# Performance work log

Measured on AMD Instinct MI355X. Metric: run time of the kernel, lower is better.

The kernel has to match this reference:

```python
import jax, jax.numpy as jnp
import numpy as np

B, T, D, L, E = 8, 2048, 256, 8, 64


def setup_inputs() -> dict:
    key = jax.random.key(0)
    ks = jax.random.split(key, 5)
    x = jax.random.normal(ks[0], (B, T, D), dtype=jnp.float32)
    # MMLP params: weight (4L, D, E), bias (4L, E); nn.Linear: (2L, D), (2L,)
    W_ml = jax.random.normal(ks[1], (4 * L, D, E), dtype=jnp.float32) * 0.05
    b_ml = jax.random.normal(ks[2], (4 * L, E), dtype=jnp.float32) * 0.05
    W_lin = jax.random.normal(ks[3], (2 * L, D), dtype=jnp.float32) * 0.05
    b_lin = jax.random.normal(ks[4], (2 * L,), dtype=jnp.float32) * 0.05
    return {"x": x, "W_ml": W_ml, "b_ml": b_ml, "W_lin": W_lin, "b_lin": b_lin}


def _xlstm_forward(x, W_ml, b_ml, W_lin, b_lin):
    b, t, _ = x.shape
    l4, _, e = W_ml.shape
    l = l4 // 4
    # Precompute all per-step gate projections at once (the torch code does this per step).
    mg = jnp.einsum('bti,lij->btlj', x, W_ml) + b_ml          # (B,T,4L,E)
    lg = jnp.einsum('bti,li->btl', x, W_lin) + b_lin          # (B,T,2L)
    o_, v, k, q = jnp.split(mg, 4, axis=2)                    # each (B,T,L,E)
    i_, f_ = jnp.split(lg, 2, axis=2)                         # each (B,T,L)
    xs = tuple(jnp.moveaxis(a, 1, 0) for a in (o_, v, k, q, i_, f_))  # time-major

    def step(carry, inp):
        m, n, C, h = carry
        o_t, v_t, k_t, q_t, i_t, f_t = inp
        m_new = jnp.maximum(f_t + m, i_t)                     # stabilizer (B,L)
        i_g = jnp.exp(i_t - m_new)
        f_g = jnp.exp(f_t + m - m_new)
        # rank-1 outer-product update of matrix cell state (B,L,E,E)
        C = f_g[:, :, None, None] * C + i_g[:, :, None, None] * (v_t[:, :, :, None] * k_t[:, :, None, :])
        n = f_g[:, :, None] * n + i_g[:, :, None] * k_t       # (B,L,E)
        denom = jnp.maximum(jnp.sum(n * q_t, axis=-1), 1.0)[:, :, None]  # clamp(.,1,inf)
        h = jax.nn.sigmoid(o_t) * jnp.einsum('blij,bli->blj', C, q_t) / denom
        return (m_new, n, C, h), None

    init = (
        jnp.zeros((b, l), jnp.float32),
        jnp.zeros((b, l, e), jnp.float32),
        jnp.zeros((b, l, e, e), jnp.float32),
        jnp.zeros((b, l, e), jnp.float32),
    )
    (m, n, C, h), _ = jax.lax.scan(step, init, xs)
    return h, C


def reference(x, W_ml, b_ml, W_lin, b_lin):
    return _xlstm_forward(x, W_ml, b_ml, W_lin, b_lin)
```

## Files before the change

kernel.cpp:

```cpp
#include <hip/hip_runtime.h>

#define B 8
#define T 2048
#define D 256
#define L 8
#define E 64
#define BT (B*T)

typedef _Float16 f16;
typedef f16 f16x8 __attribute__((ext_vector_type(8)));
typedef float f32x4 __attribute__((ext_vector_type(4)));

#define OFF_I   0
#define OFF_F   (OFF_I  + B*L*T)
#define OFF_WT  (OFF_F  + B*L*T)
#define OFF_VT  (OFF_WT + 16*E*D/2)
#define OFF_KT  (OFF_VT + B*L*E*T/2)
#define OFF_CP  (OFF_KT + B*L*E*T/2)
#define OFF_X16 (OFF_CP + 64*4*4160)

__global__ __launch_bounds__(256) void k_prep_all(const float* __restrict__ x,
        const float* __restrict__ Wlin, const float* __restrict__ blin,
        const float* __restrict__ Wml,
        float* __restrict__ ibuf, float* __restrict__ fbuf,
        f16* __restrict__ Wt16, f16* __restrict__ x16) {
    __shared__ __align__(16) char smem[49920];
    int tid = threadIdx.x;
    int bx = blockIdx.x;
    if (bx < 512) {
        float (*xs)[260] = (float(*)[260])smem;
        float (*wsm)[260] = (float(*)[260])(smem + 33280);
        int t0 = bx * 32;
        {
            int row = tid >> 3, q = tid & 7;
            const float* src = x + (size_t)(t0 + row) * D + q * 32;
            #pragma unroll
            for (int j = 0; j < 8; ++j) {
                float4 v = *(const float4*)(src + j * 4);
                *(float4*)&xs[row][q * 32 + j * 4] = v;
            }
        }
        {
            int row = tid >> 4, c0 = (tid & 15) * 16;
            const float* src = Wlin + row * D + c0;
            #pragma unroll
            for (int j = 0; j < 4; ++j) {
                float4 v = *(const float4*)(src + j * 4);
                *(float4*)&wsm[row][c0 + j * 4] = v;
            }
        }
        __syncthreads();
        int tl = tid >> 4, g = tid & 15;
        float acc0 = 0.f, acc1 = 0.f;
        for (int i = 0; i < D; ++i) {
            float wv = wsm[g][i];
            acc0 += xs[tl * 2 + 0][i] * wv;
            acc1 += xs[tl * 2 + 1][i] * wv;
        }
        float bias = blin[g];
        float acc[2] = {acc0 + bias, acc1 + bias};
        #pragma unroll
        for (int u = 0; u < 2; ++u) {
            int t = t0 + tl * 2 + u;
            int b = t >> 11, tt = t & 2047;
            if (g < 8) ibuf[(b * L + g) * T + tt] = acc[u];
            else       fbuf[(b * L + (g - 8)) * T + tt] = acc[u];
        }
    } else if (bx < 528) {
        float (*ts)[65] = (float(*)[65])smem;
        int vkrow = bx - 512;
        int wrow = 8 + vkrow;
        for (int dc = 0; dc < 4; ++dc) {
            int d0 = dc * 64;
            int r = tid >> 2, cq = (tid & 3) * 16;
            const float* src = Wml + ((size_t)wrow * D + d0 + r) * E + cq;
            #pragma unroll
            for (int j = 0; j < 16; j += 4) {
                float4 v = *(const float4*)(src + j);
                ts[r][cq + j] = v.x; ts[r][cq + j + 1] = v.y;
                ts[r][cq + j + 2] = v.z; ts[r][cq + j + 3] = v.w;
            }
            __syncthreads();
            int e = tid >> 2, dq = (tid & 3) * 16;
            f16* dst = Wt16 + ((size_t)vkrow * E + e) * D + d0 + dq;
            f16x8 o0, o1;
            #pragma unroll
            for (int j = 0; j < 8; ++j) {
                o0[j] = (f16)ts[dq + j][e];
                o1[j] = (f16)ts[dq + 8 + j][e];
            }
            *(f16x8*)dst = o0;
            *(f16x8*)(dst + 8) = o1;
            __syncthreads();
        }
    } else {
        int i = ((bx - 528) * 256 + tid) * 8;
        float4 v0 = *(const float4*)(x + i);
        float4 v1 = *(const float4*)(x + i + 4);
        f16x8 o;
        o[0] = (f16)v0.x; o[1] = (f16)v0.y; o[2] = (f16)v0.z; o[3] = (f16)v0.w;
        o[4] = (f16)v1.x; o[5] = (f16)v1.y; o[6] = (f16)v1.z; o[7] = (f16)v1.w;
        *(f16x8*)(x16 + i) = o;
    }
}

__global__ __launch_bounds__(512) void k_vkproj3(const f16* __restrict__ x16,
        const f16* __restrict__ Wt16, const float* __restrict__ bml,
        f16* __restrict__ Vt, f16* __restrict__ Kt) {
    __shared__ __align__(16) char lds[40960];
    int tid = threadIdx.x;
    int bx = blockIdx.x, h = blockIdx.y;
    int t0 = bx * 128;
    const f16* xa = x16 + (size_t)t0 * D;
    const f16* wb = Wt16 + (size_t)h * 8 * E * D;
    int wv = tid >> 6, lane = tid & 63;
    int wr = wv >> 2, wc = wv & 3;
    int q = lane >> 4, lr = lane & 15;
    int sa_t = tid >> 2, sa_q = tid & 3;
    f32x4 acc[4][8] = {};
    for (int ks = 0; ks < 8; ++ks) {
        int k0 = ks * 32;
        {
            f16x8 v = *(const f16x8*)(xa + (size_t)sa_t * D + k0 + sa_q * 8);
            int ba = sa_t * 64 + ((sa_q ^ ((sa_t >> 1) & 3)) << 4);
            *(f16x8*)(lds + ba) = v;
        }
        #pragma unroll
        for (int rr = 0; rr < 4; ++rr) {
            int r = rr * 128 + (tid >> 2);
            int c = tid & 3;
            f16x8 v = *(const f16x8*)(wb + (size_t)r * D + k0 + c * 8);
            int ba = 8192 + r * 64 + ((c ^ ((r >> 1) & 3)) << 4);
            *(f16x8*)(lds + ba) = v;
        }
        __syncthreads();
        f16x8 a[4], bf[8];
        #pragma unroll
        for (int m = 0; m < 4; ++m) {
            int t = wr * 64 + m * 16 + lr;
            int ba = t * 64 + ((q ^ ((t >> 1) & 3)) << 4);
            a[m] = *(const f16x8*)(lds + ba);
        }
        #pragma unroll
        for (int n = 0; n < 8; ++n) {
            int c = wc * 128 + n * 16 + lr;
            int ba = 8192 + c * 64 + ((q ^ ((c >> 1) & 3)) << 4);
            bf[n] = *(const f16x8*)(lds + ba);
        }
        #pragma unroll
        for (int m = 0; m < 4; ++m)
            #pragma unroll
            for (int n = 0; n < 8; ++n)
                acc[m][n] = __builtin_amdgcn_mfma_f32_16x16x32_f16(
                    a[m], bf[n], acc[m][n], 0, 0, 0);
        __syncthreads();
    }
    const float* bp = bml + (size_t)(8 + h * 8) * E;
    int b_g = t0 >> 11, tin = t0 & 2047;
    f16* obase = h ? Kt : Vt;
    for (int p = 0; p < 4; ++p) {
        if (wc == p) {
            #pragma unroll
            for (int n = 0; n < 8; ++n) {
                int cc = n * 16 + lr;
                float bias = bp[p * 128 + cc];
                int swz = (cc & 7) << 4;
                #pragma unroll
                for (int m = 0; m < 4; ++m) {
                    #pragma unroll
                    for (int r = 0; r < 4; r += 2) {
                        int t = wr * 64 + m * 16 + q * 4 + r;
                        union { f16 h2[2]; unsigned u; } pk;
                        pk.h2[0] = (f16)(acc[m][n][r] + bias);
                        pk.h2[1] = (f16)(acc[m][n][r + 1] + bias);
                        int ba = cc * 256 + ((t * 2) ^ swz);
                        *(unsigned*)(lds + ba) = pk.u;
                    }
                }
            }
        }
        __syncthreads();
        {
            int cc = tid >> 2, part = tid & 3;
            int cg = p * 128 + cc;
            int l = cg >> 6, e = cg & 63;
            f16* dst = obase + ((size_t)((b_g * L + l) * E + e)) * T + tin + part * 32;
            int swz = (cc & 7) << 4;
            #pragma unroll
            for (int jj = 0; jj < 4; ++jj) {
                int t = part * 32 + jj * 8;
                int ba = cc * 256 + ((t * 2) ^ swz);
                *(f16x8*)(dst + jj * 8) = *(const f16x8*)(lds + ba);
            }
        }
        __syncthreads();
    }
}

__global__ __launch_bounds__(256) void k_cgemm2s(const f16* __restrict__ Vt,
        const f16* __restrict__ Kt, const float* __restrict__ ibuf,
        const float* __restrict__ fbuf, float* __restrict__ Cpart) {
    __shared__ float red[64 * 64];
    __shared__ float redn[64];
    __shared__ float part[256];
    __shared__ float rmax[256];
    __shared__ __align__(16) f16 wlds[512];
    int tid = threadIdx.x;
    int bl = blockIdx.x, tc = blockIdx.y;
    int wv = tid >> 6, lane = tid & 63;
    {
        const float* fp = fbuf + bl * T + tid * 8;
        const float* ip = ibuf + bl * T + tid * 8;
        float4 fa = *(const float4*)fp;
        float4 fb = *(const float4*)(fp + 4);
        float4 ia = *(const float4*)ip;
        float4 ib = *(const float4*)(ip + 4);
        float f[8] = {fa.x, fa.y, fa.z, fa.w, fb.x, fb.y, fb.z, fb.w};
        float iv[8] = {ia.x, ia.y, ia.z, ia.w, ib.x, ib.y, ib.z, ib.w};
        float ls[8]; float run = 0.f;
        #pragma unroll
        for (int r = 0; r < 8; ++r) { run += f[r]; ls[r] = run; }
        part[tid] = run;
        __syncthreads();
        float inc = run;
        #pragma unroll
        for (int s = 1; s < 256; s <<= 1) {
            float u = (tid >= s) ? part[tid - s] : 0.f;
            __syncthreads();
            inc += u;
            part[tid] = inc;
            __syncthreads();
        }
        float off = inc - run;
        float e[8]; float lmax = -1e30f;
        #pragma unroll
        for (int r = 0; r < 8; ++r) { e[r] = iv[r] - (off + ls[r]); lmax = fmaxf(lmax, e[r]); }
        rmax[tid] = lmax;
        __syncthreads();
        for (int s = 128; s > 0; s >>= 1) {
            if (tid < s) rmax[tid] = fmaxf(rmax[tid], rmax[tid + s]);
            __syncthreads();
        }
        float M = fmaxf(rmax[0], 0.0f);
        int t = tid * 8;
        if ((t >> 9) == tc) {
            f16x8 w8;
            #pragma unroll
            for (int r = 0; r < 8; ++r) w8[r] = (f16)__expf(e[r] - M);
            *(f16x8*)&wlds[t & 511] = w8;
        }
        __syncthreads();
    }
    const f16* vp = Vt + (size_t)bl * E * T;
    const f16* kp = Kt + (size_t)bl * E * T;
    f32x4 acc[5][4] = {};
    int tbase = tc * 512 + wv * 128;
    for (int kc = 0; kc < 4; ++kc) {
        int tt = tbase + kc * 32 + (lane >> 4) * 8;
        f16x8 wfrag = *(const f16x8*)&wlds[tt & 511];
        f16x8 a[5], bf[4];
        #pragma unroll
        for (int m = 0; m < 4; ++m) {
            int i = m * 16 + (lane & 15);
            f16x8 v = *(const f16x8*)(vp + (size_t)i * T + tt);
            a[m] = v * wfrag;
        }
        a[4] = wfrag;
        #pragma unroll
        for (int nn = 0; nn < 4; ++nn) {
            int j = nn * 16 + (lane & 15);
            bf[nn] = *(const f16x8*)(kp + (size_t)j * T + tt);
        }
        #pragma unroll
        for (int m = 0; m < 5; ++m)
            #pragma unroll
            for (int nn = 0; nn < 4; ++nn)
                acc[m][nn] = __builtin_amdgcn_mfma_f32_16x16x32_f16(
                    a[m], bf[nn], acc[m][nn], 0, 0, 0);
    }
    for (int rr = 0; rr < 4; ++rr) {
        if (wv == rr) {
            #pragma unroll
            for (int m = 0; m < 4; ++m)
                #pragma unroll
                for (int nn = 0; nn < 4; ++nn)
                    #pragma unroll
                    for (int r = 0; r < 4; ++r) {
                        int row = m * 16 + (lane >> 4) * 4 + r;
                        int col = nn * 16 + (lane & 15);
                        if (rr == 0) red[row * 64 + col] = acc[m][nn][r];
                        else         red[row * 64 + col] += acc[m][nn][r];
                    }
            if ((lane >> 4) == 0) {
                #pragma unroll
                for (int nn = 0; nn < 4; ++nn) {
                    int col = nn * 16 + (lane & 15);
                    if (rr == 0) redn[col] = acc[4][nn][0];
                    else         redn[col] += acc[4][nn][0];
                }
            }
        }
        __syncthreads();
    }
    float* cp = Cpart + ((size_t)bl * 4 + tc) * 4160;
    #pragma unroll
    for (int j = 0; j < 4; ++j) {
        int idx = tid * 16 + j * 4;
        *(float4*)(cp + idx) = *(const float4*)(red + idx);
    }
    if (tid < 64) cp[4096 + tid] = redn[tid];
}

__global__ __launch_bounds__(256) void k_final(const float* __restrict__ x,
        const float* __restrict__ Wml, const float* __restrict__ bml,
        const float* __restrict__ Cpart, float* __restrict__ out) {
    __shared__ float Cs[E * E];
    __shared__ float xs[D];
    __shared__ float ns[E];
    __shared__ float os[E];
    __shared__ float qs[E];
    int tid = threadIdx.x;
    int bl = blockIdx.x; int b = bl >> 3, l = bl & 7;
    xs[tid] = x[((size_t)(b * T + (T - 1))) * D + tid];
    const float* cp = Cpart + (size_t)bl * 4 * 4160;
    #pragma unroll
    for (int j = 0; j < 4; ++j) {
        int idx = tid * 16 + j * 4;
        float4 s = {0, 0, 0, 0};
        #pragma unroll
        for (int p = 0; p < 4; ++p) {
            float4 v = *(const float4*)(cp + p * 4160 + idx);
            s.x += v.x; s.y += v.y; s.z += v.z; s.w += v.w;
        }
        *(float4*)&Cs[idx] = s;
        *(float4*)(out + 4096 + (size_t)bl * (E * E) + idx) = s;
    }
    if (tid < 64) {
        float s = 0.f;
        #pragma unroll
        for (int p = 0; p < 4; ++p) s += cp[p * 4160 + 4096 + tid];
        ns[tid] = s;
    }
    __syncthreads();
    if (tid < 128) {
        int gate = tid >> 6, e = tid & 63;
        int wrow = gate ? (3 * L + l) : l;
        const float* wpp = Wml + (size_t)wrow * D * E + e;
        float s = 0.f;
        for (int kk = 0; kk < D; ++kk) s += xs[kk] * wpp[kk * E];
        s += bml[wrow * E + e];
        if (gate) qs[e] = s; else os[e] = s;
    }
    __syncthreads();
    if (tid < 64) {
        int j = tid;
        float hc = 0.f;
        for (int i2 = 0; i2 < E; ++i2) hc += Cs[i2 * E + j] * qs[i2];
        float nq = 0.f;
        for (int i2 = 0; i2 < E; ++i2) nq += ns[i2] * qs[i2];
        float denom = fmaxf(nq, 1.0f);
        float sg = 1.0f / (1.0f + __expf(-os[j]));
        out[bl * E + j] = sg * hc / denom;
    }
}

extern "C" void kernel_launch(void* const* d_in, const int* in_sizes, int n_in,
                              void* d_out, int out_size, void* d_ws, size_t ws_size,
                              hipStream_t stream) {
    const float* x    = (const float*)d_in[0];
    const float* Wml  = (const float*)d_in[1];
    const float* bml  = (const float*)d_in[2];
    const float* Wlin = (const float*)d_in[3];
    const float* blin = (const float*)d_in[4];
    float* out = (float*)d_out;
    float* ws = (float*)d_ws;
    float* ibuf  = ws + OFF_I;
    float* fbuf  = ws + OFF_F;
    f16*   Wt16  = (f16*)(ws + OFF_WT);
    f16*   Vt    = (f16*)(ws + OFF_VT);
    f16*   Kt    = (f16*)(ws + OFF_KT);
    float* Cpart = ws + OFF_CP;
    f16*   x16   = (f16*)(ws + OFF_X16);

    k_prep_all<<<2576, 256, 0, stream>>>(x, Wlin, blin, Wml, ibuf, fbuf, Wt16, x16);
    k_vkproj3<<<dim3(BT / 128, 2), 512, 0, stream>>>(x16, Wt16, bml, Vt, Kt);
    k_cgemm2s<<<dim3(B * L, 4), 256, 0, stream>>>(Vt, Kt, ibuf, fbuf, Cpart);
    k_final<<<B * L, 256, 0, stream>>>(x, Wml, bml, Cpart, out);
}
```

Before: 65.34 us.

## Fuse four kernels into one cooperative persistent kernel with grid syncs

Replaces the four-kernel pipeline (prep, V/K projection GEMM, chunked C GEMM, final reduction) with a single cooperative launch of 256 blocks of 512 threads, separated by grid-wide syncs. The o/q projection for the final step moves into the prep phase. The scan and C-GEMM phase is reorganised for 512 threads. The aim is to remove kernel launch gaps and tail effects across the small stages. In exchange it adds grid-barrier costs and fixes the occupancy to 256 blocks, which may underuse the GPU in the prep and GEMM phases.

Result: slower. 188.0 us (+187.7%).

```diff
diff --git a/kernel.cpp b/kernel.cpp
--- a/kernel.cpp
+++ b/kernel.cpp
@@ -1,4 +1,6 @@
 #include <hip/hip_runtime.h>
+#include <hip/hip_cooperative_groups.h>
+namespace cg = cooperative_groups;
 
 #define B 8
 #define T 2048
@@ -18,349 +20,361 @@
 #define OFF_KT  (OFF_VT + B*L*E*T/2)
 #define OFF_CP  (OFF_KT + B*L*E*T/2)
 #define OFF_X16 (OFF_CP + 64*4*4160)
-
-__global__ __launch_bounds__(256) void k_prep_all(const float* __restrict__ x,
-        const float* __restrict__ Wlin, const float* __restrict__ blin,
-        const float* __restrict__ Wml,
+#define OFF_OQ  (OFF_X16 + BT*D/2)
+
+__global__ __launch_bounds__(512, 2) void k_mega(
+        const float* __restrict__ x, const float* __restrict__ Wml,
+        const float* __restrict__ bml, const float* __restrict__ Wlin,
+        const float* __restrict__ blin, float* __restrict__ out,
         float* __restrict__ ibuf, float* __restrict__ fbuf,
-        f16* __restrict__ Wt16, f16* __restrict__ x16) {
+        f16* __restrict__ Wt16, f16* __restrict__ Vt, f16* __restrict__ Kt,
+        float* __restrict__ Cpart, f16* __restrict__ x16,
+        float* __restrict__ oqbuf) {
     __shared__ __align__(16) char smem[49920];
+    cg::grid_group grid = cg::this_grid();
     int tid = threadIdx.x;
-    int bx = blockIdx.x;
-    if (bx < 512) {
+    int bid = blockIdx.x;
+
+    {
         float (*xs)[260] = (float(*)[260])smem;
-        float (*wsm)[260] = (float(*)[260])(smem + 33280);
-        int t0 = bx * 32;
+        float (*wl)[260] = (float(*)[260])(smem + 33280);
         {
-            int row = tid >> 3, q = tid & 7;
-            const float* src = x + (size_t)(t0 + row) * D + q * 32;
-            #pragma unroll
-            for (int j = 0; j < 8; ++j) {
-                float4 v = *(const float4*)(src + j * 4);
-                *(float4*)&xs[row][q * 32 + j * 4] = v;
-            }
-        }
-        {
-            int row = tid >> 4, c0 = (tid & 15) * 16;
-            const float* src = Wlin + row * D + c0;
-            #pragma unroll
-            for (int j = 0; j < 4; ++j) {
-                float4 v = *(const float4*)(src + j * 4);
-                *(float4*)&wsm[row][c0 + j * 4] = v;
-            }
-        }
-        __syncthreads();
-        int tl = tid >> 4, g = tid & 15;
-        float acc0 = 0.f, acc1 = 0.f;
-        for (int i = 0; i < D; ++i) {
-            float wv = wsm[g][i];
-            acc0 += xs[tl * 2 + 0][i] * wv;
-            acc1 += xs[tl * 2 + 1][i] * wv;
-        }
-        float bias = blin[g];
-        float acc[2] = {acc0 + bias, acc1 + bias};
+            int row = tid >> 5, c = (tid & 31) * 8;
+            const float* src = Wlin + row * D + c;
+            float4 v0 = *(const float4*)src, v1 = *(const float4*)(src + 4);
+            *(float4*)&wl[row][c] = v0; *(float4*)&wl[row][c + 4] = v1;
+        }
         #pragma unroll
         for (int u = 0; u < 2; ++u) {
-            int t = t0 + tl * 2 + u;
-            int b = t >> 11, tt = t & 2047;
-            if (g < 8) ibuf[(b * L + g) * T + tt] = acc[u];
-            else       fbuf[(b * L + (g - 8)) * T + tt] = acc[u];
-        }
-    } else if (bx < 528) {
-        float (*ts)[65] = (float(*)[65])smem;
-        int vkrow = bx - 512;
-        int wrow = 8 + vkrow;
-        for (int dc = 0; dc < 4; ++dc) {
-            int d0 = dc * 64;
-            int r = tid >> 2, cq = (tid & 3) * 16;
+            int t0 = bid * 64 + u * 32;
+            int row = tid >> 4, q = (tid & 15) * 16;
+            const float* src = x + (size_t)(t0 + row) * D + q;
+            float4 a0 = *(const float4*)src;
+            float4 a1 = *(const float4*)(src + 4);
+            float4 a2 = *(const float4*)(src + 8);
+            float4 a3 = *(const float4*)(src + 12);
+            __syncthreads();
+            *(float4*)&xs[row][q] = a0;
+            *(float4*)&xs[row][q + 4] = a1;
+            *(float4*)&xs[row][q + 8] = a2;
+            *(float4*)&xs[row][q + 12] = a3;
+            f16x8 h0, h1;
+            h0[0]=(f16)a0.x; h0[1]=(f16)a0.y; h0[2]=(f16)a0.z; h0[3]=(f16)a0.w;
+            h0[4]=(f16)a1.x; h0[5]=(f16)a1.y; h0[6]=(f16)a1.z; h0[7]=(f16)a1.w;
+            h1[0]=(f16)a2.x; h1[1]=(f16)a2.y; h1[2]=(f16)a2.z; h1[3]=(f16)a2.w;
+            h1[4]=(f16)a3.x; h1[5]=(f16)a3.y; h1[6]=(f16)a3.z; h1[7]=(f16)a3.w;
+            *(f16x8*)(x16 + (size_t)(t0 + row) * D + q) = h0;
+            *(f16x8*)(x16 + (size_t)(t0 + row) * D + q + 8) = h1;
+            __syncthreads();
+            int tt = tid >> 4, g = tid & 15;
+            float acc = 0.f;
+            for (int d = 0; d < D; d += 4) {
+                float4 xv = *(const float4*)&xs[tt][d];
+                float4 wv = *(const float4*)&wl[g][d];
+                acc += xv.x * wv.x + xv.y * wv.y + xv.z * wv.z + xv.w * wv.w;
+            }
+            acc += blin[g];
+            int t = t0 + tt; int b = t >> 11, trem = t & 2047;
+            if (g < 8) ibuf[(b * L + g) * T + trem] = acc;
+            else       fbuf[(b * L + (g - 8)) * T + trem] = acc;
+        }
+        if (bid < 64) {
+            __syncthreads();
+            float (*ts)[65] = (float(*)[65])smem;
+            int vkrow = bid >> 2, dc = bid & 3;
+            int wrow = 8 + vkrow, d0 = dc * 64;
+            int r = tid >> 3, cq = (tid & 7) * 8;
             const float* src = Wml + ((size_t)wrow * D + d0 + r) * E + cq;
-            #pragma unroll
-            for (int j = 0; j < 16; j += 4) {
-                float4 v = *(const float4*)(src + j);
-                ts[r][cq + j] = v.x; ts[r][cq + j + 1] = v.y;
-                ts[r][cq + j + 2] = v.z; ts[r][cq + j + 3] = v.w;
-            }
-            __syncthreads();
-            int e = tid >> 2, dq = (tid & 3) * 16;
-            f16* dst = Wt16 + ((size_t)vkrow * E + e) * D + d0 + dq;
-            f16x8 o0, o1;
-            #pragma unroll
-            for (int j = 0; j < 8; ++j) {
-                o0[j] = (f16)ts[dq + j][e];
-                o1[j] = (f16)ts[dq + 8 + j][e];
-            }
-            *(f16x8*)dst = o0;
-            *(f16x8*)(dst + 8) = o1;
-            __syncthreads();
-        }
-    } else {
-        int i = ((bx - 528) * 256 + tid) * 8;
-        float4 v0 = *(const float4*)(x + i);
-        float4 v1 = *(const float4*)(x + i + 4);
-        f16x8 o;
-        o[0] = (f16)v0.x; o[1] = (f16)v0.y; o[2] = (f16)v0.z; o[3] = (f16)v0.w;
-        o[4] = (f16)v1.x; o[5] = (f16)v1.y; o[6] = (f16)v1.z; o[7] = (f16)v1.w;
-        *(f16x8*)(x16 + i) = o;
+            float4 v0 = *(const float4*)src, v1 = *(const float4*)(src + 4);
+            *(float4*)&ts[r][cq] = v0; *(float4*)&ts[r][cq + 4] = v1;
+            __syncthreads();
+            int e = tid >> 3, dq = (tid & 7) * 8;
+            f16x8 o;
+            #pragma unroll
+            for (int j = 0; j < 8; ++j) o[j] = (f16)ts[dq + j][e];
+            *(f16x8*)(Wt16 + ((size_t)vkrow * E + e) * D + d0 + dq) = o;
+        } else if (bid < 72) {
+            __syncthreads();
+            float (*x8)[256] = (float(*)[256])smem;
+            int l = bid - 64;
+            {
+                int bb = tid >> 6, c = (tid & 63) * 4;
+                float4 v = *(const float4*)(x + ((size_t)(bb * T + (T - 1))) * D + c);
+                *(float4*)&x8[bb][c] = v;
+            }
+            __syncthreads();
+            #pragma unroll
+            for (int r = 0; r < 2; ++r) {
+                int idx = r * 512 + tid;
+                int gate = idx >> 9, b = (idx >> 6) & 7, e = idx & 63;
+                int row = gate ? (24 + l) : l;
+                const float* gp = Wml + (size_t)row * D * E + e;
+                float s = 0.f;
+                for (int kk = 0; kk < D; ++kk) s += x8[b][kk] * gp[(size_t)kk * E];
+                s += bml[row * E + e];
+                oqbuf[(b * L + l) * 128 + gate * 64 + e] = s;
+            }
+        }
     }
-}
-
-__global__ __launch_bounds__(512) void k_vkproj3(const f16* __restrict__ x16,
-        const f16* __restrict__ Wt16, const float* __restrict__ bml,
-        f16* __restrict__ Vt, f16* __restrict__ Kt) {
-    __shared__ __align__(16) char lds[40960];
-    int tid = threadIdx.x;
-    int bx = blockIdx.x, h = blockIdx.y;
-    int t0 = bx * 128;
-    const f16* xa = x16 + (size_t)t0 * D;
-    const f16* wb = Wt16 + (size_t)h * 8 * E * D;
-    int wv = tid >> 6, lane = tid & 63;
-    int wr = wv >> 2, wc = wv & 3;
-    int q = lane >> 4, lr = lane & 15;
-    int sa_t = tid >> 2, sa_q = tid & 3;
-    f32x4 acc[4][8] = {};
-    for (int ks = 0; ks < 8; ++ks) {
-        int k0 = ks * 32;
-        {
-            f16x8 v = *(const f16x8*)(xa + (size_t)sa_t * D + k0 + sa_q * 8);
-            int ba = sa_t * 64 + ((sa_q ^ ((sa_t >> 1) & 3)) << 4);
-            *(f16x8*)(lds + ba) = v;
-        }
-        #pragma unroll
-        for (int rr = 0; rr < 4; ++rr) {
-            int r = rr * 128 + (tid >> 2);
-            int c = tid & 3;
-            f16x8 v = *(const f16x8*)(wb + (size_t)r * D + k0 + c * 8);
-            int ba = 8192 + r * 64 + ((c ^ ((r >> 1) & 3)) << 4);
-            *(f16x8*)(lds + ba) = v;
-        }
-        __syncthreads();
-        f16x8 a[4], bf[8];
-        #pragma unroll
-        for (int m = 0; m < 4; ++m) {
-            int t = wr * 64 + m * 16 + lr;
-            int ba = t * 64 + ((q ^ ((t >> 1) & 3)) << 4);
-            a[m] = *(const f16x8*)(lds + ba);
-        }
-        #pragma unroll
-        for (int n = 0; n < 8; ++n) {
-            int c = wc * 128 + n * 16 + lr;
-            int ba = 8192 + c * 64 + ((q ^ ((c >> 1) & 3)) << 4);
-            bf[n] = *(const f16x8*)(lds + ba);
-        }
-        #pragma unroll
-        for (int m = 0; m < 4; ++m)
-            #pragma unroll
-            for (int n = 0; n < 8; ++n)
-                acc[m][n] = __builtin_amdgcn_mfma_f32_16x16x32_f16(
-                    a[m], bf[n], acc[m][n], 0, 0, 0);
-        __syncthreads();
-    }
-    const float* bp = bml + (size_t)(8 + h * 8) * E;
-    int b_g = t0 >> 11, tin = t0 & 2047;
-    f16* obase = h ? Kt : Vt;
-    for (int p = 0; p < 4; ++p) {
-        if (wc == p) {
+    grid.sync();
+
+    {
+        char* lds = smem;
+        int bx = bid & 127, h = bid >> 7;
+        int t0 = bx * 128;
+        const f16* xa = x16 + (size_t)t0 * D;
+        const f16* wb = Wt16 + (size_t)h * 8 * E * D;
+        int wv = tid >> 6, lane = tid & 63;
+        int wr = wv >> 2, wc = wv & 3;
+        int q = lane >> 4, lr = lane & 15;
+        int sa_t = tid >> 2, sa_q = tid & 3;
+        f32x4 acc[4][8] = {};
+        for (int ks = 0; ks < 8; ++ks) {
+            int k0 = ks * 32;
+            {
+                f16x8 v = *(const f16x8*)(xa + (size_t)sa_t * D + k0 + sa_q * 8);
+                int ba = sa_t * 64 + ((sa_q ^ ((sa_t >> 1) & 3)) << 4);
+                *(f16x8*)(lds + ba) = v;
+            }
+            #pragma unroll
+            for (int rr = 0; rr < 4; ++rr) {
+                int r = rr * 128 + (tid >> 2);
+                int c = tid & 3;
+                f16x8 v = *(const f16x8*)(wb + (size_t)r * D + k0 + c * 8);
+                int ba = 8192 + r * 64 + ((c ^ ((r >> 1) & 3)) << 4);
+                *(f16x8*)(lds + ba) = v;
+            }
+            __syncthreads();
+            f16x8 a[4], bf[8];
+            #pragma unroll
+            for (int m = 0; m < 4; ++m) {
+                int t = wr * 64 + m * 16 + lr;
+                int ba = t * 64 + ((q ^ ((t >> 1) & 3)) << 4);
+                a[m] = *(const f16x8*)(lds + ba);
+            }
             #pragma unroll
             for (int n = 0; n < 8; ++n) {
-                int cc = n * 16 + lr;
-                float bias = bp[p * 128 + cc];
-                int swz = (cc & 7) << 4;
-                #pragma unroll
-                for (int m = 0; m < 4; ++m) {
+                int c = wc * 128 + n * 16 + lr;
+                int ba = 8192 + c * 64 + ((q ^ ((c >> 1) & 3)) << 4);
+                bf[n] = *(const f16x8*)(lds + ba);
+            }
+            #pragma unroll
+            for (int m = 0; m < 4; ++m)
+                #pragma unroll
+                for (int n = 0; n < 8; ++n)
+                    acc[m][n] = __builtin_amdgcn_mfma_f32_16x16x32_f16(
+                        a[m], bf[n], acc[m][n], 0, 0, 0);
+            __syncthreads();
+        }
+        const float* bp = bml + (size_t)(8 + h * 8) * E;
+        int b_g = t0 >> 11, tin = t0 & 2047;
+        f16* obase = h ? Kt : Vt;
+        for (int p = 0; p < 4; ++p) {
+            if (wc == p) {
+                #pragma unroll
+                for (int n = 0; n < 8; ++n) {
+                    int cc = n * 16 + lr;
+                    float bias = bp[p * 128 + cc];
+                    int swz = (cc & 7) << 4;
                     #pragma unroll
-                    for (int r = 0; r < 4; r += 2) {
-                        int t = wr * 64 + m * 16 + q * 4 + r;
-                        union { f16 h2[2]; unsigned u; } pk;
-                        pk.h2[0] = (f16)(acc[m][n][r] + bias);
-                        pk.h2[1] = (f16)(acc[m][n][r + 1] + bias);
-                        int ba = cc * 256 + ((t * 2) ^ swz);
-                        *(unsigned*)(lds + ba) = pk.u;
+                    for (int m = 0; m < 4; ++m) {
+                        #pragma unroll
+                        for (int r = 0; r < 4; r += 2) {
+                            int t = wr * 64 + m * 16 + q * 4 + r;
+                            union { f16 h2[2]; unsigned u; } pk;
+                            pk.h2[0] = (f16)(acc[m][n][r] + bias);
+                            pk.h2[1] = (f16)(acc[m][n][r + 1] + bias);
+                            int ba = cc * 256 + ((t * 2) ^ swz);
+                            *(unsigned*)(lds + ba) = pk.u;
+                        }
                     }
                 }
             }
-        }
-        __syncthreads();
+            __syncthreads();
+            {
+                int cc = tid >> 2, part = tid & 3;
+                int cg2 = p * 128 + cc;
+                int l = cg2 >> 6, e = cg2 & 63;
+                f16* dst = obase + ((size_t)((b_g * L + l) * E + e)) * T + tin + part * 32;
+                int swz = (cc & 7) << 4;
+                #pragma unroll
+                for (int jj = 0; jj < 4; ++jj) {
+                    int t = part * 32 + jj * 8;
+                    int ba = cc * 256 + ((t * 2) ^ swz);
+                    *(f16x8*)(dst + jj * 8) = *(const f16x8*)(lds + ba);
+                }
+            }
+            __syncthreads();
+        }
+    }
+    grid.sync();
+
+    {
+        int bl = bid >> 2, tc = bid & 3;
+        float* red0  = (float*)smem;
+        float* red1  = (float*)(smem + 16384);
+        float* part  = (float*)(smem + 32768);
+        float* rmax  = (float*)(smem + 34816);
+        f16*   wlds  = (f16*)(smem + 36864);
+        float* redn0 = (float*)(smem + 37888);
+        float* redn1 = (float*)(smem + 38144);
         {
-            int cc = tid >> 2, part = tid & 3;
-            int cg = p * 128 + cc;
-            int l = cg >> 6, e = cg & 63;
-            f16* dst = obase + ((size_t)((b_g * L + l) * E + e)) * T + tin + part * 32;
-            int swz = (cc & 7) << 4;
-            #pragma unroll
-            for (int jj = 0; jj < 4; ++jj) {
-                int t = part * 32 + jj * 8;
-                int ba = cc * 256 + ((t * 2) ^ swz);
-                *(f16x8*)(dst + jj * 8) = *(const f16x8*)(lds + ba);
-            }
-        }
-        __syncthreads();
+            const float* fp = fbuf + bl * T + tid * 4;
+            const float* ip = ibuf + bl * T + tid * 4;
+            float4 fa = *(const float4*)fp;
+            float4 ia = *(const float4*)ip;
+            float f0[4] = {fa.x, fa.y, fa.z, fa.w};
+            float iv[4] = {ia.x, ia.y, ia.z, ia.w};
+            float ls[4]; float run = 0.f;
+            #pragma unroll
+            for (int r = 0; r < 4; ++r) { run += f0[r]; ls[r] = run; }
+            part[tid] = run;
+            __syncthreads();
+            float inc = run;
+            #pragma unroll
+            for (int s = 1; s < 512; s <<= 1) {
+                float uu = (tid >= s) ? part[tid - s] : 0.f;
+                __syncthreads();
+                inc += uu;
+                part[tid] = inc;
+                __syncthreads();
+            }
+            float off = inc - run;
+            float e[4]; float lmax = -1e30f;
+            #pragma unroll
+            for (int r = 0; r < 4; ++r) { e[r] = iv[r] - (off + ls[r]); lmax = fmaxf(lmax, e[r]); }
+            rmax[tid] = lmax;
+            __syncthreads();
+            for (int s = 256; s > 0; s >>= 1) {
+                if (tid < s) rmax[tid] = fmaxf(rmax[tid], rmax[tid + s]);
+                __syncthreads();
+            }
+            float M = fmaxf(rmax[0], 0.0f);
+            int tg = tid * 4;
+            if ((tg >> 9) == tc) {
+                union { f16 h[4]; unsigned long long u; } pw;
+                #pragma unroll
+                for (int r = 0; r < 4; ++r) pw.h[r] = (f16)__expf(e[r] - M);
+                *(unsigned long long*)&wlds[tg & 511] = pw.u;
+            }
+            __syncthreads();
+        }
+        int wv = tid >> 6, lane = tid & 63;
+        const f16* vp = Vt + (size_t)bl * E * T;
+        const f16* kp = Kt + (size_t)bl * E * T;
+        f32x4 acc[5][4] = {};
+        int tw = tc * 512 + wv * 64;
+        #pragma unroll
+        for (int kc = 0; kc < 2; ++kc) {
+            int lo = wv * 64 + kc * 32 + (lane >> 4) * 8;
+            int tt = tc * 512 + lo;
+            f16x8 wfrag = *(const f16x8*)&wlds[lo];
+            f16x8 a[5], bf[4];
+            #pragma unroll
+            for (int m = 0; m < 4; ++m) {
+                int i = m * 16 + (lane & 15);
+                f16x8 v = *(const f16x8*)(vp + (size_t)i * T + tt);
+                a[m] = v * wfrag;
+            }
+            a[4] = wfrag;
+            #pragma unroll
+            for (int nn = 0; nn < 4; ++nn) {
+                int j = nn * 16 + (lane & 15);
+                bf[nn] = *(const f16x8*)(kp + (size_t)j * T + tt);
+            }
+            #pragma unroll
+            for (int m = 0; m < 5; ++m)
+                #pragma unroll
+                for (int nn = 0; nn < 4; ++nn)
+                    acc[m][nn] = __builtin_amdgcn_mfma_f32_16x16x32_f16(
+                        a[m], bf[nn], acc[m][nn], 0, 0, 0);
+        }
+        (void)tw;
+        for (int rr = 0; rr < 4; ++rr) {
+            if (wv == rr || wv == rr + 4) {
+                float* rd = (wv < 4) ? red0 : red1;
+                float* rn = (wv < 4) ? redn0 : redn1;
+                #pragma unroll
+                for (int m = 0; m < 4; ++m)
+                    #pragma unroll
+                    for (int nn = 0; nn < 4; ++nn)
+                        #pragma unroll
+                        for (int r = 0; r < 4; ++r) {
+                            int row = m * 16 + (lane >> 4) * 4 + r;
+                            int col = nn * 16 + (lane & 15);
+                            if (rr == 0) rd[row * 64 + col] = acc[m][nn][r];
+                            else         rd[row * 64 + col] += acc[m][nn][r];
+                        }
+                if ((lane >> 4) == 0) {
+                    #pragma unroll
+                    for (int nn = 0; nn < 4; ++nn) {
+                        int col = nn * 16 + (lane & 15);
+                        if (rr == 0) rn[col] = acc[4][nn][0];
+                        else         rn[col] += acc[4][nn][0];
+                    }
+                }
+            }
+            __syncthreads();
+        }
+        float* cp = Cpart + ((size_t)bl * 4 + tc) * 4160;
+        int idx = tid * 8;
+        float4 s0, s1;
+        {
+            float4 a0 = *(const float4*)(red0 + idx);
+            float4 b0 = *(const float4*)(red1 + idx);
+            float4 a1 = *(const float4*)(red0 + idx + 4);
+            float4 b1 = *(const float4*)(red1 + idx + 4);
+            s0.x = a0.x + b0.x; s0.y = a0.y + b0.y; s0.z = a0.z + b0.z; s0.w = a0.w + b0.w;
+            s1.x = a1.x + b1.x; s1.y = a1.y + b1.y; s1.z = a1.z + b1.z; s1.w = a1.w + b1.w;
+        }
+        *(float4*)(cp + idx) = s0;
+        *(float4*)(cp + idx + 4) = s1;
+        if (tid < 64) cp[4096 + tid] = redn0[tid] + redn1[tid];
     }
-}
-
-__global__ __launch_bounds__(256) void k_cgemm2s(const f16* __restrict__ Vt,
-        const f16* __restrict__ Kt, const float* __restrict__ ibuf,
-        const float* __restrict__ fbuf, float* __restrict__ Cpart) {
-    __shared__ float red[64 * 64];
-    __shared__ float redn[64];
-    __shared__ float part[256];
-    __shared__ float rmax[256];
-    __shared__ __align__(16) f16 wlds[512];
-    int tid = threadIdx.x;
-    int bl = blockIdx.x, tc = blockIdx.y;
-    int wv = tid >> 6, lane = tid & 63;
-    {
-        const float* fp = fbuf + bl * T + tid * 8;
-        const float* ip = ibuf + bl * T + tid * 8;
-        float4 fa = *(const float4*)fp;
-        float4 fb = *(const float4*)(fp + 4);
-        float4 ia = *(const float4*)ip;
-        float4 ib = *(const float4*)(ip + 4);
-        float f[8] = {fa.x, fa.y, fa.z, fa.w, fb.x, fb.y, fb.z, fb.w};
-        float iv[8] = {ia.x, ia.y, ia.z, ia.w, ib.x, ib.y, ib.z, ib.w};
-        float ls[8]; float run = 0.f;
-        #pragma unroll
-        for (int r = 0; r < 8; ++r) { run += f[r]; ls[r] = run; }
-        part[tid] = run;
-        __syncthreads();
-        float inc = run;
-        #pragma unroll
-        for (int s = 1; s < 256; s <<= 1) {
-            float u = (tid >= s) ? part[tid - s] : 0.f;
-            __syncthreads();
-            inc += u;
-            part[tid] = inc;
-            __syncthreads();
-        }
-        float off = inc - run;
-        float e[8]; float lmax = -1e30f;
-        #pragma unroll
-        for (int r = 0; r < 8; ++r) { e[r] = iv[r] - (off + ls[r]); lmax = fmaxf(lmax, e[r]); }
-        rmax[tid] = lmax;
-        __syncthreads();
-        for (int s = 128; s > 0; s >>= 1) {
-            if (tid < s) rmax[tid] = fmaxf(rmax[tid], rmax[tid + s]);
-            __syncthreads();
-        }
-        float M = fmaxf(rmax[0], 0.0f);
-        int t = tid * 8;
-        if ((t >> 9) == tc) {
-            f16x8 w8;
-            #pragma unroll
-            for (int r = 0; r < 8; ++r) w8[r] = (f16)__expf(e[r] - M);
-            *(f16x8*)&wlds[t & 511] = w8;
-        }
-        __syncthreads();
-    }
-    const f16* vp = Vt + (size_t)bl * E * T;
-    const f16* kp = Kt + (size_t)bl * E * T;
-    f32x4 acc[5][4] = {};
-    int tbase = tc * 512 + wv * 128;
-    for (int kc = 0; kc < 4; ++kc) {
-        int tt = tbase + kc * 32 + (lane >> 4) * 8;
-        f16x8 wfrag = *(const f16x8*)&wlds[tt & 511];
-        f16x8 a[5], bf[4];
-        #pragma unroll
-        for (int m = 0; m < 4; ++m) {
-            int i = m * 16 + (lane & 15);
-            f16x8 v = *(const f16x8*)(vp + (size_t)i * T + tt);
-            a[m] = v * wfrag;
-        }
-        a[4] = wfrag;
-        #pragma unroll
-        for (int nn = 0; nn < 4; ++nn) {
-            int j = nn * 16 + (lane & 15);
-            bf[nn] = *(const f16x8*)(kp + (size_t)j * T + tt);
-        }
-        #pragma unroll
-        for (int m = 0; m < 5; ++m)
-            #pragma unroll
-            for (int nn = 0; nn < 4; ++nn)
-                acc[m][nn] = __builtin_amdgcn_mfma_f32_16x16x32_f16(
-                    a[m], bf[nn], acc[m][nn], 0, 0, 0);
-    }
-    for (int rr = 0; rr < 4; ++rr) {
-        if (wv == rr) {
-            #pragma unroll
-            for (int m = 0; m < 4; ++m)
-                #pragma unroll
-                for (int nn = 0; nn < 4; ++nn)
-                    #pragma unroll
-                    for (int r = 0; r < 4; ++r) {
-                        int row = m * 16 + (lane >> 4) * 4 + r;
-                        int col = nn * 16 + (lane & 15);
-                        if (rr == 0) red[row * 64 + col] = acc[m][nn][r];
-                        else         red[row * 64 + col] += acc[m][nn][r];
-                    }
-            if ((lane >> 4) == 0) {
-                #pragma unroll
-                for (int nn = 0; nn < 4; ++nn) {
-                    int col = nn * 16 + (lane & 15);
-                    if (rr == 0) redn[col] = acc[4][nn][0];
-                    else         redn[col] += acc[4][nn][0];
-                }
-            }
-        }
-        __syncthreads();
-    }
-    float* cp = Cpart + ((size_t)bl * 4 + tc) * 4160;
-    #pragma unroll
-    for (int j = 0; j < 4; ++j) {
-        int idx = tid * 16 + j * 4;
-        *(float4*)(cp + idx) = *(const float4*)(red + idx);
-    }
-    if (tid < 64) cp[4096 + tid] = redn[tid];
-}
-
-__global__ __launch_bounds__(256) void k_final(const float* __restrict__ x,
-        const float* __restrict__ Wml, const float* __restrict__ bml,
-        const float* __restrict__ Cpart, float* __restrict__ out) {
-    __shared__ float Cs[E * E];
-    __shared__ float xs[D];
-    __shared__ float ns[E];
-    __shared__ float os[E];
-    __shared__ float qs[E];
-    int tid = threadIdx.x;
-    int bl = blockIdx.x; int b = bl >> 3, l = bl & 7;
-    xs[tid] = x[((size_t)(b * T + (T - 1))) * D + tid];
-    const float* cp = Cpart + (size_t)bl * 4 * 4160;
-    #pragma unroll
-    for (int j = 0; j < 4; ++j) {
-        int idx = tid * 16 + j * 4;
-        float4 s = {0, 0, 0, 0};
+    grid.sync();
+
+    if (bid < 64) {
+        int bl = bid;
+        float* Cs  = (float*)smem;
+        float* ns  = (float*)(smem + 16384);
+        float* osb = (float*)(smem + 16640);
+        float* qsb = (float*)(smem + 16896);
+        const float* cp = Cpart + (size_t)bl * 4 * 4160;
+        int idx = tid * 8;
+        float4 s0 = {0,0,0,0}, s1 = {0,0,0,0};
         #pragma unroll
         for (int p = 0; p < 4; ++p) {
-            float4 v = *(const float4*)(cp + p * 4160 + idx);
-            s.x += v.x; s.y += v.y; s.z += v.z; s.w += v.w;
-        }
-        *(float4*)&Cs[idx] = s;
-        *(float4*)(out + 4096 + (size_t)bl * (E * E) + idx) = s;
-    }
-    if (tid < 64) {
-        float s = 0.f;
-        #pragma unroll
-        for (int p = 0; p < 4; ++p) s += cp[p * 4160 + 4096 + tid];
-        ns[tid] = s;
-    }
-    __syncthreads();
-    if (tid < 128) {
-        int gate = tid >> 6, e = tid & 63;
-        int wrow = gate ? (3 * L + l) : l;
-        const float* wpp = Wml + (size_t)wrow * D * E + e;
-        float s = 0.f;
-        for (int kk = 0; kk < D; ++kk) s += xs[kk] * wpp[kk * E];
-        s += bml[wrow * E + e];
-        if (gate) qs[e] = s; else os[e] = s;
-    }
-    __syncthreads();
-    if (tid < 64) {
-        int j = tid;
-        float hc = 0.f;
-        for (int i2 = 0; i2 < E; ++i2) hc += Cs[i2 * E + j] * qs[i2];
-        float nq = 0.f;
-        for (int i2 = 0; i2 < E; ++i2) nq += ns[i2] * qs[i2];
-        float denom = fmaxf(nq, 1.0f);
-        float sg = 1.0f / (1.0f + __expf(-os[j]));
-        out[bl * E + j] = sg * hc / denom;
+            float4 v0 = *(const float4*)(cp + p * 4160 + idx);
+            float4 v1 = *(const float4*)(cp + p * 4160 + idx + 4);
+            s0.x += v0.x; s0.y += v0.y; s0.z += v0.z; s0.w += v0.w;
+            s1.x += v1.x; s1.y += v1.y; s1.z += v1.z; s1.w += v1.w;
+        }
+        *(float4*)&Cs[idx] = s0;
+        *(float4*)&Cs[idx + 4] = s1;
+        *(float4*)(out + 4096 + (size_t)bl * 4096 + idx) = s0;
+        *(float4*)(out + 4096 + (size_t)bl * 4096 + idx + 4) = s1;
+        if (tid < 64) {
+            float s = 0.f;
+            #pragma unroll
+            for (int p = 0; p < 4; ++p) s += cp[p * 4160 + 4096 + tid];
+            ns[tid] = s;
+        }
+        if (tid < 128) {
+            float v = oqbuf[bl * 128 + tid];
+            if (tid < 64) osb[tid] = v; else qsb[tid - 64] = v;
+        }
+        __syncthreads();
+        if (tid < 64) {
+            int j = tid;
+            float hc = 0.f, nq = 0.f;
+            for (int i2 = 0; i2 < E; ++i2) {
+                hc += Cs[i2 * 64 + j] * qsb[i2];
+                nq += ns[i2] * qsb[i2];
+            }
+            float denom = fmaxf(nq, 1.0f);
+            float sg = 1.0f / (1.0f + __expf(-osb[j]));
+            out[bl * 64 + j] = sg * hc / denom;
+        }
     }
 }
 
@@ -381,9 +395,13 @@
     f16*   Kt    = (f16*)(ws + OFF_KT);
     float* Cpart = ws + OFF_CP;
     f16*   x16   = (f16*)(ws + OFF_X16);
-
-    k_prep_all<<<2576, 256, 0, stream>>>(x, Wlin, blin, Wml, ibuf, fbuf, Wt16, x16);
-    k_vkproj3<<<dim3(BT / 128, 2), 512, 0, stream>>>(x16, Wt16, bml, Vt, Kt);
-    k_cgemm2s<<<dim3(B * L, 4), 256, 0, stream>>>(Vt, Kt, ibuf, fbuf, Cpart);
-    k_final<<<B * L, 256, 0, stream>>>(x, Wml, bml, Cpart, out);
+    float* oqbuf = ws + OFF_OQ;
+
+    void* args[] = {
+        (void*)&x, (void*)&Wml, (void*)&bml, (void*)&Wlin, (void*)&blin,
+        (void*)&out, (void*)&ibuf, (void*)&fbuf, (void*)&Wt16,
+        (void*)&Vt, (void*)&Kt, (void*)&Cpart, (void*)&x16, (void*)&oqbuf
+    };
+    hipLaunchCooperativeKernel((void*)k_mega, dim3(256), dim3(512),
+                               args, 0, stream);
 }
```

## Fuse final readout into C-GEMM kernel and fold x16 conversion into prep

Applied to the files above, without the earlier changes.

Folds the fp16 conversion of x into the i/f-gate projection blocks, so the separate conversion blocks that re-read x are gone. The o/q projections for the last timestep move into 8 extra prep blocks. The separate final kernel is merged into the C-GEMM kernel, which now uses 64 blocks of 512 threads, each covering all of T, instead of 256 blocks writing partial sums to workspace. This removes one launch and the partial-sum round trip. In exchange the GEMM stage runs far fewer blocks on a large GPU, so each block does more serial work.

New measurement: 76.88 us. 17.7% more time.

```diff
diff --git a/kernel.cpp b/kernel.cpp
--- a/kernel.cpp
+++ b/kernel.cpp
@@ -16,14 +16,15 @@
 #define OFF_WT  (OFF_F  + B*L*T)
 #define OFF_VT  (OFF_WT + 16*E*D/2)
 #define OFF_KT  (OFF_VT + B*L*E*T/2)
-#define OFF_CP  (OFF_KT + B*L*E*T/2)
-#define OFF_X16 (OFF_CP + 64*4*4160)
-
-__global__ __launch_bounds__(256) void k_prep_all(const float* __restrict__ x,
+#define OFF_X16 (OFF_KT + B*L*E*T/2)
+#define OFF_OQ  (OFF_X16 + BT*D/2)
+
+__global__ __launch_bounds__(256) void k_prep(const float* __restrict__ x,
         const float* __restrict__ Wlin, const float* __restrict__ blin,
-        const float* __restrict__ Wml,
+        const float* __restrict__ Wml, const float* __restrict__ bml,
         float* __restrict__ ibuf, float* __restrict__ fbuf,
-        f16* __restrict__ Wt16, f16* __restrict__ x16) {
+        f16* __restrict__ Wt16, f16* __restrict__ x16,
+        float* __restrict__ oqbuf) {
     __shared__ __align__(16) char smem[49920];
     int tid = threadIdx.x;
     int bx = blockIdx.x;
@@ -32,12 +33,19 @@
         float (*wsm)[260] = (float(*)[260])(smem + 33280);
         int t0 = bx * 32;
         {
-            int row = tid >> 3, q = tid & 7;
-            const float* src = x + (size_t)(t0 + row) * D + q * 32;
-            #pragma unroll
-            for (int j = 0; j < 8; ++j) {
-                float4 v = *(const float4*)(src + j * 4);
-                *(float4*)&xs[row][q * 32 + j * 4] = v;
+            int row = tid >> 3, q = (tid & 7) * 32;
+            const float* src = x + (size_t)(t0 + row) * D + q;
+            f16* xdst = x16 + (size_t)(t0 + row) * D + q;
+            #pragma unroll
+            for (int j = 0; j < 4; ++j) {
+                float4 v0 = *(const float4*)(src + j * 8);
+                float4 v1 = *(const float4*)(src + j * 8 + 4);
+                *(float4*)&xs[row][q + j * 8] = v0;
+                *(float4*)&xs[row][q + j * 8 + 4] = v1;
+                f16x8 h;
+                h[0]=(f16)v0.x; h[1]=(f16)v0.y; h[2]=(f16)v0.z; h[3]=(f16)v0.w;
+                h[4]=(f16)v1.x; h[5]=(f16)v1.y; h[6]=(f16)v1.z; h[7]=(f16)v1.w;
+                *(f16x8*)(xdst + j * 8) = h;
             }
         }
         {
@@ -94,13 +102,27 @@
             __syncthreads();
         }
     } else {
-        int i = ((bx - 528) * 256 + tid) * 8;
-        float4 v0 = *(const float4*)(x + i);
-        float4 v1 = *(const float4*)(x + i + 4);
-        f16x8 o;
-        o[0] = (f16)v0.x; o[1] = (f16)v0.y; o[2] = (f16)v0.z; o[3] = (f16)v0.w;
-        o[4] = (f16)v1.x; o[5] = (f16)v1.y; o[6] = (f16)v1.z; o[7] = (f16)v1.w;
-        *(f16x8*)(x16 + i) = o;
+        float (*x8)[256] = (float(*)[256])smem;
+        int l = bx - 528;
+        {
+            int bb = tid >> 5, c = (tid & 31) * 8;
+            const float* src = x + ((size_t)(bb * T + (T - 1))) * D + c;
+            float4 v0 = *(const float4*)src, v1 = *(const float4*)(src + 4);
+            *(float4*)&x8[bb][c] = v0;
+            *(float4*)&x8[bb][c + 4] = v1;
+        }
+        __syncthreads();
+        #pragma unroll
+        for (int r = 0; r < 4; ++r) {
+            int idx = r * 256 + tid;
+            int gate = idx >> 9, b = (idx >> 6) & 7, e = idx & 63;
+            int row = gate ? (24 + l) : l;
+            const float* gp = Wml + (size_t)row * D * E + e;
+            float s = 0.f;
+            for (int kk = 0; kk < D; ++kk) s += x8[b][kk] * gp[(size_t)kk * E];
+            s += bml[row * E + e];
+            oqbuf[(b * L + l) * 128 + gate * 64 + e] = s;
+        }
     }
 }
 
@@ -182,8 +204,8 @@
         __syncthreads();
         {
             int cc = tid >> 2, part = tid & 3;
-            int cg = p * 128 + cc;
-            int l = cg >> 6, e = cg & 63;
+            int cg2 = p * 128 + cc;
+            int l = cg2 >> 6, e = cg2 & 63;
             f16* dst = obase + ((size_t)((b_g * L + l) * E + e)) * T + tin + part * 32;
             int swz = (cc & 7) << 4;
             #pragma unroll
@@ -197,67 +219,66 @@
     }
 }
 
-__global__ __launch_bounds__(256) void k_cgemm2s(const f16* __restrict__ Vt,
+__global__ __launch_bounds__(512) void k_cgemm_final(const f16* __restrict__ Vt,
         const f16* __restrict__ Kt, const float* __restrict__ ibuf,
-        const float* __restrict__ fbuf, float* __restrict__ Cpart) {
-    __shared__ float red[64 * 64];
-    __shared__ float redn[64];
-    __shared__ float part[256];
-    __shared__ float rmax[256];
-    __shared__ __align__(16) f16 wlds[512];
+        const float* __restrict__ fbuf, const float* __restrict__ oqbuf,
+        float* __restrict__ out) {
+    __shared__ __align__(16) char smem[41984];
+    float* red0  = (float*)smem;
+    float* red1  = (float*)(smem + 16384);
+    float* part  = (float*)(smem + 32768);
+    float* rmax  = (float*)(smem + 34816);
+    f16*   wlds  = (f16*)(smem + 36864);
+    float* redn0 = (float*)(smem + 40960);
+    float* redn1 = (float*)(smem + 41216);
     int tid = threadIdx.x;
-    int bl = blockIdx.x, tc = blockIdx.y;
+    int bl = blockIdx.x;
     int wv = tid >> 6, lane = tid & 63;
     {
-        const float* fp = fbuf + bl * T + tid * 8;
-        const float* ip = ibuf + bl * T + tid * 8;
+        const float* fp = fbuf + bl * T + tid * 4;
+        const float* ip = ibuf + bl * T + tid * 4;
         float4 fa = *(const float4*)fp;
-        float4 fb = *(const float4*)(fp + 4);
         float4 ia = *(const float4*)ip;
-        float4 ib = *(const float4*)(ip + 4);
-        float f[8] = {fa.x, fa.y, fa.z, fa.w, fb.x, fb.y, fb.z, fb.w};
-        float iv[8] = {ia.x, ia.y, ia.z, ia.w, ib.x, ib.y, ib.z, ib.w};
-        float ls[8]; float run = 0.f;
-        #pragma unroll
-        for (int r = 0; r < 8; ++r) { run += f[r]; ls[r] = run; }
+        float f0[4] = {fa.x, fa.y, fa.z, fa.w};
+        float iv[4] = {ia.x, ia.y, ia.z, ia.w};
+        float ls[4]; float run = 0.f;
+        #pragma unroll
+        for (int r = 0; r < 4; ++r) { run += f0[r]; ls[r] = run; }
         part[tid] = run;
         __syncthreads();
         float inc = run;
         #pragma unroll
-        for (int s = 1; s < 256; s <<= 1) {
-            float u = (tid >= s) ? part[tid - s] : 0.f;
-            __syncthreads();
-            inc += u;
+        for (int s = 1; s < 512; s <<= 1) {
+            float uu = (tid >= s) ? part[tid - s] : 0.f;
+            __syncthreads();
+            inc += uu;
             part[tid] = inc;
             __syncthreads();
         }
         float off = inc - run;
-        float e[8]; float lmax = -1e30f;
-        #pragma unroll
-        for (int r = 0; r < 8; ++r) { e[r] = iv[r] - (off + ls[r]); lmax = fmaxf(lmax, e[r]); }
+        float e[4]; float lmax = -1e30f;
+        #pragma unroll
+        for (int r = 0; r < 4; ++r) { e[r] = iv[r] - (off + ls[r]); lmax = fmaxf(lmax, e[r]); }
         rmax[tid] = lmax;
         __syncthreads();
-        for (int s = 128; s > 0; s >>= 1) {
+        for (int s = 256; s > 0; s >>= 1) {
             if (tid < s) rmax[tid] = fmaxf(rmax[tid], rmax[tid + s]);
             __syncthreads();
         }
         float M = fmaxf(rmax[0], 0.0f);
-        int t = tid * 8;
-        if ((t >> 9) == tc) {
-            f16x8 w8;
-            #pragma unroll
-            for (int r = 0; r < 8; ++r) w8[r] = (f16)__expf(e[r] - M);
-            *(f16x8*)&wlds[t & 511] = w8;
-        }
+        union { f16 h[4]; unsigned long long u; } pw;
+        #pragma unroll
+        for (int r = 0; r < 4; ++r) pw.h[r] = (f16)__expf(e[r] - M);
+        *(unsigned long long*)&wlds[tid * 4] = pw.u;
         __syncthreads();
     }
     const f16* vp = Vt + (size_t)bl * E * T;
     const f16* kp = Kt + (size_t)bl * E * T;
     f32x4 acc[5][4] = {};
-    int tbase = tc * 512 + wv * 128;
-    for (int kc = 0; kc < 4; ++kc) {
-        int tt = tbase + kc * 32 + (lane >> 4) * 8;
-        f16x8 wfrag = *(const f16x8*)&wlds[tt & 511];
+    #pragma unroll
+    for (int kc = 0; kc < 8; ++kc) {
+        int tt = wv * 256 + kc * 32 + (lane >> 4) * 8;
+        f16x8 wfrag = *(const f16x8*)&wlds[tt];
         f16x8 a[5], bf[4];
         #pragma unroll
         for (int m = 0; m < 4; ++m) {
@@ -279,7 +300,9 @@
                     a[m], bf[nn], acc[m][nn], 0, 0, 0);
     }
     for (int rr = 0; rr < 4; ++rr) {
-        if (wv == rr) {
+        if (wv == rr || wv == rr + 4) {
+            float* rd = (wv < 4) ? red0 : red1;
+            float* rn = (wv < 4) ? redn0 : redn1;
             #pragma unroll
             for (int m = 0; m < 4; ++m)
                 #pragma unroll
@@ -288,79 +311,47 @@
                     for (int r = 0; r < 4; ++r) {
                         int row = m * 16 + (lane >> 4) * 4 + r;
                         int col = nn * 16 + (lane & 15);
-                        if (rr == 0) red[row * 64 + col] = acc[m][nn][r];
-                        else         red[row * 64 + col] += acc[m][nn][r];
+                        if (rr == 0) rd[row * 64 + col] = acc[m][nn][r];
+                        else         rd[row * 64 + col] += acc[m][nn][r];
                     }
             if ((lane >> 4) == 0) {
                 #pragma unroll
                 for (int nn = 0; nn < 4; ++nn) {
                     int col = nn * 16 + (lane & 15);
-                    if (rr == 0) redn[col] = acc[4][nn][0];
-                    else         redn[col] += acc[4][nn][0];
+                    if (rr == 0) rn[col] = acc[4][nn][0];
+                    else         rn[col] += acc[4][nn][0];
                 }
             }
         }
         __syncthreads();
     }
-    float* cp = Cpart + ((size_t)bl * 4 + tc) * 4160;
-    #pragma unroll
-    for (int j = 0; j < 4; ++j) {
-        int idx = tid * 16 + j * 4;
-        *(float4*)(cp + idx) = *(const float4*)(red + idx);
-    }
-    if (tid < 64) cp[4096 + tid] = redn[tid];
-}
-
-__global__ __launch_bounds__(256) void k_final(const float* __restrict__ x,
-        const float* __restrict__ Wml, const float* __restrict__ bml,
-        const float* __restrict__ Cpart, float* __restrict__ out) {
-    __shared__ float Cs[E * E];
-    __shared__ float xs[D];
-    __shared__ float ns[E];
-    __shared__ float os[E];
-    __shared__ float qs[E];
-    int tid = threadIdx.x;
-    int bl = blockIdx.x; int b = bl >> 3, l = bl & 7;
-    xs[tid] = x[((size_t)(b * T + (T - 1))) * D + tid];
-    const float* cp = Cpart + (size_t)bl * 4 * 4160;
-    #pragma unroll
-    for (int j = 0; j < 4; ++j) {
-        int idx = tid * 16 + j * 4;
-        float4 s = {0, 0, 0, 0};
-        #pragma unroll
-        for (int p = 0; p < 4; ++p) {
-            float4 v = *(const float4*)(cp + p * 4160 + idx);
-            s.x += v.x; s.y += v.y; s.z += v.z; s.w += v.w;
-        }
-        *(float4*)&Cs[idx] = s;
-        *(float4*)(out + 4096 + (size_t)bl * (E * E) + idx) = s;
-    }
-    if (tid < 64) {
-        float s = 0.f;
-        #pragma unroll
-        for (int p = 0; p < 4; ++p) s += cp[p * 4160 + 4096 + tid];
-        ns[tid] = s;
-    }
-    __syncthreads();
-    if (tid < 128) {
-        int gate = tid >> 6, e = tid & 63;
-        int wrow = gate ? (3 * L + l) : l;
-        const float* wpp = Wml + (size_t)wrow * D * E + e;
-        float s = 0.f;
-        for (int kk = 0; kk < D; ++kk) s += xs[kk] * wpp[kk * E];
-        s += bml[wrow * E + e];
-        if (gate) qs[e] = s; else os[e] = s;
+    {
+        int idx = tid * 8;
+        float4 a0 = *(const float4*)(red0 + idx);
+        float4 b0 = *(const float4*)(red1 + idx);
+        float4 a1 = *(const float4*)(red0 + idx + 4);
+        float4 b1 = *(const float4*)(red1 + idx + 4);
+        float4 s0 = {a0.x + b0.x, a0.y + b0.y, a0.z + b0.z, a0.w + b0.w};
+        float4 s1 = {a1.x + b1.x, a1.y + b1.y, a1.z + b1.z, a1.w + b1.w};
+        *(float4*)(out + 4096 + (size_t)bl * 4096 + idx) = s0;
+        *(float4*)(out + 4096 + (size_t)bl * 4096 + idx + 4) = s1;
+        *(float4*)(red0 + idx) = s0;
+        *(float4*)(red0 + idx + 4) = s1;
+        if (tid < 64) redn0[tid] = redn0[tid] + redn1[tid];
     }
     __syncthreads();
     if (tid < 64) {
         int j = tid;
-        float hc = 0.f;
-        for (int i2 = 0; i2 < E; ++i2) hc += Cs[i2 * E + j] * qs[i2];
-        float nq = 0.f;
-        for (int i2 = 0; i2 < E; ++i2) nq += ns[i2] * qs[i2];
+        float hc = 0.f, nq = 0.f;
+        const float* oq = oqbuf + bl * 128;
+        for (int i2 = 0; i2 < E; ++i2) {
+            float qv = oq[64 + i2];
+            hc += red0[i2 * 64 + j] * qv;
+            nq += redn0[i2] * qv;
+        }
         float denom = fmaxf(nq, 1.0f);
-        float sg = 1.0f / (1.0f + __expf(-os[j]));
-        out[bl * E + j] = sg * hc / denom;
+        float sg = 1.0f / (1.0f + __expf(-oq[j]));
+        out[bl * 64 + j] = sg * hc / denom;
     }
 }
 
@@ -379,11 +370,11 @@
     f16*   Wt16  = (f16*)(ws + OFF_WT);
     f16*   Vt    = (f16*)(ws + OFF_VT);
     f16*   Kt    = (f16*)(ws + OFF_KT);
-    float* Cpart = ws + OFF_CP;
     f16*   x16   = (f16*)(ws + OFF_X16);
-
-    k_prep_all<<<2576, 256, 0, stream>>>(x, Wlin, blin, Wml, ibuf, fbuf, Wt16, x16);
+    float* oqbuf = ws + OFF_OQ;
+
+    k_prep<<<536, 256, 0, stream>>>(x, Wlin, blin, Wml, bml,
+                                    ibuf, fbuf, Wt16, x16, oqbuf);
     k_vkproj3<<<dim3(BT / 128, 2), 512, 0, stream>>>(x16, Wt16, bml, Vt, Kt);
-    k_cgemm2s<<<dim3(B * L, 4), 256, 0, stream>>>(Vt, Kt, ibuf, fbuf, Cpart);
-    k_final<<<B * L, 256, 0, stream>>>(x, Wml, bml, Cpart, out);
+    k_cgemm_final<<<B * L, 512, 0, stream>>>(Vt, Kt, ibuf, fbuf, oqbuf, out);
 }
```
